# Optimization experiments

Hardware: AMD Instinct MI355X
Metric: run time of the kernel (lower is better)

## Reference

```python
import jax, jax.numpy as jnp
import numpy as np

EMBED_DIM = 128
BATCH = 8
SEQ = 2048


def setup_inputs() -> dict:
    key = jax.random.key(0)
    k1, k2, k3 = jax.random.split(key, 3)
    inputs = jax.random.normal(k1, (BATCH, SEQ, EMBED_DIM), dtype=jnp.float32)
    rotation_params = jax.random.normal(k2, (EMBED_DIM * 3,), dtype=jnp.float32)
    entangle_params = jax.random.normal(k3, (EMBED_DIM,), dtype=jnp.float32)
    return {"inputs": inputs, "rotation_params": rotation_params, "entangle_params": entangle_params}


def reference(inputs, rotation_params, entangle_params):
    d = inputs.shape[-1]
    rot = rotation_params.reshape(d, 3)          # [d, 3]
    ent = entangle_params.reshape(d, 1)          # [d, 1]
    query = inputs @ rot                         # [B, S, 3]
    key = inputs @ ent                           # [B, S, 1]
    # scores: [B, S, S], softmax over last axis
    logits = jnp.einsum('bsk,btk->bst', query, key) / jnp.sqrt(jnp.float32(d))
    scores = jax.nn.softmax(logits, axis=-1)
    return jnp.einsum('bst,btd->bsd', scores, inputs)  # [B, S, d]
```

## Files before the change

### kernel.cpp

```cpp
#include <hip/hip_runtime.h>
#include <cstddef>
#include <cstdint>

#define SS 2048
#define DD 128
#define NB 8

typedef _Float16 half8 __attribute__((ext_vector_type(8)));
typedef __fp16 fp16x2 __attribute__((ext_vector_type(2)));
typedef __attribute__((ext_vector_type(16))) float f32x16;

#if __has_builtin(__builtin_amdgcn_exp2f)
#define EXP2F(x) __builtin_amdgcn_exp2f(x)
#else
#define EXP2F(x) exp2f(x)
#endif

#define WS_A2   0
#define WS_KV   (NB*SS*4)
#define WS_XF   (2*NB*SS*4)
#define BATCH_B (SS*DD*2)
#define WS_NEED (size_t)(WS_XF + (size_t)NB*BATCH_B)
#define WS_KMX  (WS_XF)
#define WS_KMN  (WS_XF + 128)


__global__ __launch_bounds__(256) void prep(
    const float* __restrict__ X, const float* __restrict__ rotp,
    const float* __restrict__ entp, uint8_t* __restrict__ ws, int do_x) {
  __shared__ __align__(16) uint8_t lbuf[128 * 80];
  const int blk = blockIdx.x;
  const int b = blk & 7;
  const int rc = blk >> 3;
  const int tid = threadIdx.x;
  const int d4 = (tid & 31) * 4;
  float* a2out = (float*)(ws + WS_A2);
  float* kout = (float*)(ws + WS_KV);

  const float4 f0 = *reinterpret_cast<const float4*>(rotp + d4 * 3);
  const float4 f1 = *reinterpret_cast<const float4*>(rotp + d4 * 3 + 4);
  const float4 f2 = *reinterpret_cast<const float4*>(rotp + d4 * 3 + 8);
  const float rs0 = f0.x + f0.y + f0.z;
  const float rs1 = f0.w + f1.x + f1.y;
  const float rs2 = f1.z + f1.w + f2.x;
  const float rs3 = f2.y + f2.z + f2.w;
  const float4 e4 = *reinterpret_cast<const float4*>(entp + d4);

#pragma unroll
  for (int rnd = 0; rnd < 4; ++rnd) {
    const int t31 = rnd * 8 + (tid >> 5);
    const int tg = rc * 32 + t31;
    const float4 xv =
        *reinterpret_cast<const float4*>(X + ((size_t)b * SS + tg) * DD + d4);
    float av = xv.x * rs0 + xv.y * rs1 + xv.z * rs2 + xv.w * rs3;
    float kv = xv.x * e4.x + xv.y * e4.y + xv.z * e4.z + xv.w * e4.w;
#pragma unroll
    for (int off = 16; off > 0; off >>= 1) {
      av += __shfl_xor(av, off, 64);
      kv += __shfl_xor(kv, off, 64);
    }
    if ((tid & 31) == 0) {
      a2out[b * SS + tg] = av * (0.08838834764831845f * 1.4426950408889634f);
      kout[b * SS + tg] = kv;
    }
    if (do_x) {
      const float vv[4] = {xv.x, xv.y, xv.z, xv.w};
#pragma unroll
      for (int i = 0; i < 4; ++i)
        *reinterpret_cast<_Float16*>(lbuf + (d4 + i) * 80 + t31 * 2) =
            (_Float16)vv[i];
    }
  }

  if (do_x) {
    __syncthreads();
    const int T = rc >> 2;
    const int wfb = (rc & 3) * 2;
    uint8_t* outb = ws + WS_XF + (size_t)b * BATCH_B + (T * 8 + wfb) * 4096;
    const int nt = tid >> 6;
    const int lane = tid & 63;
    const int hh = lane >> 5;
    const int d = nt * 32 + (lane & 31);
#pragma unroll
    for (int wfl = 0; wfl < 2; ++wfl) {
      const half8 v = *reinterpret_cast<const half8*>(
          lbuf + d * 80 + (wfl * 16 + hh * 8) * 2);
      *reinterpret_cast<half8*>(outb + wfl * 4096 + nt * 1024 + lane * 16) = v;
    }
  }
}

__global__ __launch_bounds__(512, 4) void attn_mfma(
    const uint8_t* __restrict__ ws, float* __restrict__ out) {
  __shared__ float comb[2][32 * 128];
  __shared__ float dl[8 * 32];
  __shared__ float smx[8], smn[8];
  const int tid = threadIdx.x;
  const int w = tid >> 6;
  const int lane = tid & 63;
  const int lm = lane & 31;
  const int h = lane >> 5;
  const int blk = blockIdx.x;
  const int b = blk & 7;
  const int s0 = (blk >> 3) * 32;

  const float* a2 = (const float*)(ws + WS_A2) + b * SS;
  const float* kb = (const float*)(ws + WS_KV) + b * SS;
  const uint8_t* xf = ws + WS_XF + (size_t)b * BATCH_B;

  const float4 k4 = *reinterpret_cast<const float4*>(kb + tid * 4);
  float mx = fmaxf(fmaxf(k4.x, k4.y), fmaxf(k4.z, k4.w));
  float mn = fminf(fminf(k4.x, k4.y), fminf(k4.z, k4.w));
#pragma unroll
  for (int off = 32; off > 0; off >>= 1) {
    mx = fmaxf(mx, __shfl_xor(mx, off, 64));
    mn = fminf(mn, __shfl_xor(mn, off, 64));
  }
  if (lane == 0) { smx[w] = mx; smn[w] = mn; }
  const float ga = a2[s0 + lm];
  __syncthreads();
  mx = smx[0]; mn = smn[0];
#pragma unroll
  for (int q = 1; q < 8; ++q) { mx = fmaxf(mx, smx[q]); mn = fminf(mn, smn[q]); }
  const float gm = fmaxf(ga * mx, ga * mn);
  float gden = 0.0f;

  f32x16 acc[4];
#pragma unroll
  for (int nt = 0; nt < 4; ++nt)
#pragma unroll
    for (int r = 0; r < 16; ++r) acc[nt][r] = 0.0f;

  const uint8_t* wb = xf + w * 4096 + lane * 16;
  const float* kp0 = kb + w * 16 + h * 8;

  half8 bf[4];
#pragma unroll
  for (int nt = 0; nt < 4; ++nt)
    bf[nt] = *reinterpret_cast<const half8*>(wb + nt * 1024);

  for (int T = 0; T < 16; ++T) {
    half8 bn[4];
    if (T < 15) {
      const uint8_t* nb_ = wb + (T + 1) * 32768;
#pragma unroll
      for (int nt = 0; nt < 4; ++nt)
        bn[nt] = *reinterpret_cast<const half8*>(nb_ + nt * 1024);
    }
    const float* kp = kp0 + T * 128;
    const float4 ka = *reinterpret_cast<const float4*>(kp);
    const float4 kc = *reinterpret_cast<const float4*>(kp + 4);
    const float kv8[8] = {ka.x, ka.y, ka.z, ka.w, kc.x, kc.y, kc.z, kc.w};
    float e0[8];
#pragma unroll
    for (int j = 0; j < 8; ++j) {
      e0[j] = EXP2F(fmaf(ga, kv8[j], -gm));
      gden += e0[j];
    }
    union { half8 v; fp16x2 p[4]; } wa;
#pragma unroll
    for (int q = 0; q < 4; ++q)
      wa.p[q] = __builtin_amdgcn_cvt_pkrtz(e0[2 * q], e0[2 * q + 1]);
    __builtin_amdgcn_s_setprio(1);
#pragma unroll
    for (int nt = 0; nt < 4; ++nt)
      acc[nt] = __builtin_amdgcn_mfma_f32_32x32x16_f16(wa.v, bf[nt], acc[nt], 0, 0, 0);
    __builtin_amdgcn_s_setprio(0);
#pragma unroll
    for (int nt = 0; nt < 4; ++nt) bf[nt] = bn[nt];
  }

  gden += __shfl_xor(gden, 32, 64);
  if (lane < 32) dl[w * 32 + lane] = gden;
#pragma unroll
  for (int p = 0; p < 4; ++p) {
    const int grp = w >> 2;
    if ((w & 3) == p) {
      float* cb = comb[grp];
#pragma unroll
      for (int nt = 0; nt < 4; ++nt)
#pragma unroll
        for (int r = 0; r < 16; ++r) {
          const int rr = (r & 3) + 8 * (r >> 2) + 4 * h;
          const int i0 = rr * 128 + nt * 32 + lm;
          if (p == 0) cb[i0] = acc[nt][r];
          else        cb[i0] += acc[nt][r];
        }
    }
    __syncthreads();
  }

  const int r = tid >> 4;
  const int cg = (tid & 15) * 8;
  float den = 0.0f;
#pragma unroll
  for (int q = 0; q < 8; ++q) den += dl[q * 32 + r];
  const float inv = 1.0f / den;
  float* orow = out + ((size_t)b * SS + s0 + r) * DD + cg;
#pragma unroll
  for (int q = 0; q < 2; ++q) {
    const float4 vA = *reinterpret_cast<const float4*>(&comb[0][r * 128 + cg + q * 4]);
    const float4 vB = *reinterpret_cast<const float4*>(&comb[1][r * 128 + cg + q * 4]);
    *reinterpret_cast<float4*>(orow + q * 4) =
        make_float4((vA.x + vB.x) * inv, (vA.y + vB.y) * inv,
                    (vA.z + vB.z) * inv, (vA.w + vB.w) * inv);
  }
}

__global__ __launch_bounds__(256) void kminmax(const float* __restrict__ kvec,
                                               float* __restrict__ kmx,
                                               float* __restrict__ kmn) {
  const int b = blockIdx.x;
  const int tid = threadIdx.x;
  float mx = -1e30f, mn = 1e30f;
  for (int i = tid; i < SS; i += 256) {
    const float v = kvec[b * SS + i];
    mx = fmaxf(mx, v);
    mn = fminf(mn, v);
  }
#pragma unroll
  for (int off = 32; off > 0; off >>= 1) {
    mx = fmaxf(mx, __shfl_xor(mx, off, 64));
    mn = fminf(mn, __shfl_xor(mn, off, 64));
  }
  __shared__ float smx[4], smn[4];
  const int wid = tid >> 6, lane = tid & 63;
  if (lane == 0) { smx[wid] = mx; smn[wid] = mn; }
  __syncthreads();
  if (tid == 0) {
    kmx[b] = fmaxf(fmaxf(smx[0], smx[1]), fmaxf(smx[2], smx[3]));
    kmn[b] = fminf(fminf(smn[0], smn[1]), fminf(smn[2], smn[3]));
  }
}

__global__ __launch_bounds__(256) void attn_main(
    const float* __restrict__ X, const float* __restrict__ a2,
    const float* __restrict__ kvec, const float* __restrict__ kmx,
    const float* __restrict__ kmn, float* __restrict__ out) {
  __shared__ float xs[64 * DD];
  __shared__ float wt[64 * 32];
  __shared__ float denp[8 * 32];
  const int tid = threadIdx.x;
  const int tx = tid & 15;
  const int ty = (tid >> 4) & 3;
  const int tz = tid >> 6;
  const int b = blockIdx.y;
  const int s0 = blockIdx.x * 32;
  const int sg = tid & 31;
  const int tq = tid >> 5;
  const float ga = a2[b * SS + s0 + sg];
  const float gm = fmaxf(ga * kmx[b], ga * kmn[b]);
  float gden = 0.0f;
  float acc[8][8];
#pragma unroll
  for (int r = 0; r < 8; ++r)
#pragma unroll
    for (int c = 0; c < 8; ++c) acc[r][c] = 0.0f;
  const float* xb = X + (size_t)b * SS * DD;
  const float* kb = kvec + b * SS;
  for (int t0 = 0; t0 < SS; t0 += 64) {
    __syncthreads();
#pragma unroll
    for (int rnd = 0; rnd < 8; ++rnd) {
      const int idx = rnd * 1024 + tid * 4;
      *reinterpret_cast<float4*>(xs + idx) =
          *reinterpret_cast<const float4*>(xb + t0 * DD + idx);
    }
#pragma unroll
    for (int j = 0; j < 8; ++j) {
      const float kt = kb[t0 + tq * 8 + j];
      const float wv = exp2f(fmaf(ga, kt, -gm));
      wt[(tq * 8 + j) * 32 + sg] = wv;
      gden += wv;
    }
    __syncthreads();
#pragma unroll 4
    for (int ti = 0; ti < 16; ++ti) {
      const int tl = tz * 16 + ti;
      const float4 x0 = *reinterpret_cast<const float4*>(xs + tl * DD + tx * 8);
      const float4 x1 = *reinterpret_cast<const float4*>(xs + tl * DD + tx * 8 + 4);
      const float4 w0 = *reinterpret_cast<const float4*>(wt + tl * 32 + ty * 8);
      const float4 w1 = *reinterpret_cast<const float4*>(wt + tl * 32 + ty * 8 + 4);
      const float xr[8] = {x0.x, x0.y, x0.z, x0.w, x1.x, x1.y, x1.z, x1.w};
      const float wr[8] = {w0.x, w0.y, w0.z, w0.w, w1.x, w1.y, w1.z, w1.w};
#pragma unroll
      for (int r = 0; r < 8; ++r)
#pragma unroll
        for (int c = 0; c < 8; ++c) acc[r][c] = fmaf(wr[r], xr[c], acc[r][c]);
    }
  }
  __syncthreads();
  denp[tq * 32 + sg] = gden;
  for (int p = 1; p < 4; ++p) {
    __syncthreads();
    if (tz == p) {
#pragma unroll
      for (int r = 0; r < 8; ++r) {
        const int sl = ty * 8 + r;
        *reinterpret_cast<float4*>(xs + sl * DD + tx * 8) =
            make_float4(acc[r][0], acc[r][1], acc[r][2], acc[r][3]);
        *reinterpret_cast<float4*>(xs + sl * DD + tx * 8 + 4) =
            make_float4(acc[r][4], acc[r][5], acc[r][6], acc[r][7]);
      }
    }
    __syncthreads();
    if (tz == 0) {
#pragma unroll
      for (int r = 0; r < 8; ++r) {
        const int sl = ty * 8 + r;
        const float4 v0 = *reinterpret_cast<const float4*>(xs + sl * DD + tx * 8);
        const float4 v1 = *reinterpret_cast<const float4*>(xs + sl * DD + tx * 8 + 4);
        acc[r][0] += v0.x; acc[r][1] += v0.y; acc[r][2] += v0.z; acc[r][3] += v0.w;
        acc[r][4] += v1.x; acc[r][5] += v1.y; acc[r][6] += v1.z; acc[r][7] += v1.w;
      }
    }
  }
  if (tz == 0) {
#pragma unroll
    for (int r = 0; r < 8; ++r) {
      const int sl = ty * 8 + r;
      float den = 0.0f;
#pragma unroll
      for (int q = 0; q < 8; ++q) den += denp[q * 32 + sl];
      const float inv = 1.0f / den;
      float* orow = out + ((size_t)b * SS + s0 + sl) * DD + tx * 8;
      *reinterpret_cast<float4*>(orow) =
          make_float4(acc[r][0] * inv, acc[r][1] * inv, acc[r][2] * inv, acc[r][3] * inv);
      *reinterpret_cast<float4*>(orow + 4) =
          make_float4(acc[r][4] * inv, acc[r][5] * inv, acc[r][6] * inv, acc[r][7] * inv);
    }
  }
}

extern "C" void kernel_launch(void* const* d_in, const int* in_sizes, int n_in,
                              void* d_out, int out_size, void* d_ws, size_t ws_size,
                              hipStream_t stream) {
  const float* X = (const float*)d_in[0];
  const float* rotp = (const float*)d_in[1];
  const float* entp = (const float*)d_in[2];
  float* out = (float*)d_out;
  uint8_t* ws = (uint8_t*)d_ws;

  if (ws_size >= WS_NEED) {
    prep<<<512, 256, 0, stream>>>(X, rotp, entp, ws, 1);
    attn_mfma<<<512, 512, 0, stream>>>((const uint8_t*)ws, out);
  } else {
    float* a2 = (float*)(ws + WS_A2);
    float* kv = (float*)(ws + WS_KV);
    float* kmxp = (float*)(ws + WS_KMX);
    float* kmnp = (float*)(ws + WS_KMN);
    prep<<<512, 256, 0, stream>>>(X, rotp, entp, ws, 0);
    kminmax<<<NB, 256, 0, stream>>>(kv, kmxp, kmnp);
    attn_main<<<dim3(SS / 32, NB), 256, 0, stream>>>(X, a2, kv, kmxp, kmnp, out);
  }
}
```

Measured before the change: 28.46 us.

## Process 64 query rows per block with 16 waves and ping-pong B buffers

The attention kernel now uses 1024-thread blocks that each cover 64 query rows, split as two 32-row halves times eight key-split waves, with half as many blocks. The eight key-split waves for each row half are reduced in one shared buffer instead of two partial buffers summed at the end. The main loop is unrolled by two with alternating A/B fragment registers, so the register-rotation copies go away. Larger blocks mean fewer blocks per CU, longer serial reduction (8 sync steps), and a launch bound of 1024 threads that may limit register allocation.

```diff
diff --git a/kernel.cpp b/kernel.cpp
--- a/kernel.cpp
+++ b/kernel.cpp
@@ -90,38 +90,40 @@
   }
 }
 
-__global__ __launch_bounds__(512, 4) void attn_mfma(
+__global__ __launch_bounds__(1024, 4) void attn_mfma(
     const uint8_t* __restrict__ ws, float* __restrict__ out) {
-  __shared__ float comb[2][32 * 128];
-  __shared__ float dl[8 * 32];
-  __shared__ float smx[8], smn[8];
+  __shared__ float comb[64 * 128];
+  __shared__ float dl[16 * 32];
+  __shared__ float smx[16], smn[16];
   const int tid = threadIdx.x;
   const int w = tid >> 6;
   const int lane = tid & 63;
   const int lm = lane & 31;
   const int h = lane >> 5;
+  const int mh = w >> 3;
+  const int ks = w & 7;
   const int blk = blockIdx.x;
   const int b = blk & 7;
-  const int s0 = (blk >> 3) * 32;
+  const int s0 = (blk >> 3) * 64;
 
   const float* a2 = (const float*)(ws + WS_A2) + b * SS;
   const float* kb = (const float*)(ws + WS_KV) + b * SS;
   const uint8_t* xf = ws + WS_XF + (size_t)b * BATCH_B;
 
-  const float4 k4 = *reinterpret_cast<const float4*>(kb + tid * 4);
-  float mx = fmaxf(fmaxf(k4.x, k4.y), fmaxf(k4.z, k4.w));
-  float mn = fminf(fminf(k4.x, k4.y), fminf(k4.z, k4.w));
+  const float2 k2 = *reinterpret_cast<const float2*>(kb + tid * 2);
+  float mx = fmaxf(k2.x, k2.y);
+  float mn = fminf(k2.x, k2.y);
 #pragma unroll
   for (int off = 32; off > 0; off >>= 1) {
     mx = fmaxf(mx, __shfl_xor(mx, off, 64));
     mn = fminf(mn, __shfl_xor(mn, off, 64));
   }
   if (lane == 0) { smx[w] = mx; smn[w] = mn; }
-  const float ga = a2[s0 + lm];
+  const float ga = a2[s0 + mh * 32 + lm];
   __syncthreads();
   mx = smx[0]; mn = smn[0];
 #pragma unroll
-  for (int q = 1; q < 8; ++q) { mx = fmaxf(mx, smx[q]); mn = fminf(mn, smn[q]); }
+  for (int q = 1; q < 16; ++q) { mx = fmaxf(mx, smx[q]); mn = fminf(mn, smn[q]); }
   const float gm = fmaxf(ga * mx, ga * mn);
   float gden = 0.0f;
 
@@ -131,60 +133,59 @@
 #pragma unroll
     for (int r = 0; r < 16; ++r) acc[nt][r] = 0.0f;
 
-  const uint8_t* wb = xf + w * 4096 + lane * 16;
-  const float* kp0 = kb + w * 16 + h * 8;
-
-  half8 bf[4];
+  const uint8_t* wb = xf + ks * 4096 + lane * 16;
+  const float* kp0 = kb + ks * 16 + h * 8;
+
+  half8 bfA[4], bfB[4];
 #pragma unroll
   for (int nt = 0; nt < 4; ++nt)
-    bf[nt] = *reinterpret_cast<const half8*>(wb + nt * 1024);
-
-  for (int T = 0; T < 16; ++T) {
-    half8 bn[4];
-    if (T < 15) {
-      const uint8_t* nb_ = wb + (T + 1) * 32768;
-#pragma unroll
-      for (int nt = 0; nt < 4; ++nt)
-        bn[nt] = *reinterpret_cast<const half8*>(nb_ + nt * 1024);
-    }
-    const float* kp = kp0 + T * 128;
-    const float4 ka = *reinterpret_cast<const float4*>(kp);
-    const float4 kc = *reinterpret_cast<const float4*>(kp + 4);
-    const float kv8[8] = {ka.x, ka.y, ka.z, ka.w, kc.x, kc.y, kc.z, kc.w};
-    float e0[8];
-#pragma unroll
-    for (int j = 0; j < 8; ++j) {
-      e0[j] = EXP2F(fmaf(ga, kv8[j], -gm));
-      gden += e0[j];
-    }
-    union { half8 v; fp16x2 p[4]; } wa;
-#pragma unroll
-    for (int q = 0; q < 4; ++q)
-      wa.p[q] = __builtin_amdgcn_cvt_pkrtz(e0[2 * q], e0[2 * q + 1]);
-    __builtin_amdgcn_s_setprio(1);
-#pragma unroll
-    for (int nt = 0; nt < 4; ++nt)
-      acc[nt] = __builtin_amdgcn_mfma_f32_32x32x16_f16(wa.v, bf[nt], acc[nt], 0, 0, 0);
-    __builtin_amdgcn_s_setprio(0);
-#pragma unroll
-    for (int nt = 0; nt < 4; ++nt) bf[nt] = bn[nt];
-  }
+    bfA[nt] = *reinterpret_cast<const half8*>(wb + nt * 1024);
+
+#define ABODY(TT, BFP, BFN)                                                   \
+  {                                                                           \
+    if ((TT) + 1 < 16) {                                                      \
+      const uint8_t* nb_ = wb + ((TT) + 1) * 32768;                           \
+      _Pragma("unroll") for (int nt = 0; nt < 4; ++nt)                        \
+          BFN[nt] = *reinterpret_cast<const half8*>(nb_ + nt * 1024);         \
+    }                                                                         \
+    const float* kp = kp0 + (TT) * 128;                                       \
+    const float4 ka = *reinterpret_cast<const float4*>(kp);                   \
+    const float4 kc = *reinterpret_cast<const float4*>(kp + 4);               \
+    const float kv8[8] = {ka.x, ka.y, ka.z, ka.w, kc.x, kc.y, kc.z, kc.w};    \
+    float e0[8];                                                              \
+    _Pragma("unroll") for (int j = 0; j < 8; ++j) {                           \
+      e0[j] = EXP2F(fmaf(ga, kv8[j], -gm));                                   \
+      gden += e0[j];                                                          \
+    }                                                                         \
+    union { half8 v; fp16x2 p[4]; } wa;                                       \
+    _Pragma("unroll") for (int q = 0; q < 4; ++q)                             \
+        wa.p[q] = __builtin_amdgcn_cvt_pkrtz(e0[2 * q], e0[2 * q + 1]);       \
+    __builtin_amdgcn_s_setprio(1);                                            \
+    _Pragma("unroll") for (int nt = 0; nt < 4; ++nt)                          \
+        acc[nt] = __builtin_amdgcn_mfma_f32_32x32x16_f16(wa.v, BFP[nt],       \
+                                                         acc[nt], 0, 0, 0);   \
+    __builtin_amdgcn_s_setprio(0);                                            \
+  }
+
+  for (int T = 0; T < 16; T += 2) {
+    ABODY(T, bfA, bfB);
+    ABODY(T + 1, bfB, bfA);
+  }
+#undef ABODY
 
   gden += __shfl_xor(gden, 32, 64);
   if (lane < 32) dl[w * 32 + lane] = gden;
 #pragma unroll
-  for (int p = 0; p < 4; ++p) {
-    const int grp = w >> 2;
-    if ((w & 3) == p) {
-      float* cb = comb[grp];
+  for (int p = 0; p < 8; ++p) {
+    if (ks == p) {
 #pragma unroll
       for (int nt = 0; nt < 4; ++nt)
 #pragma unroll
         for (int r = 0; r < 16; ++r) {
           const int rr = (r & 3) + 8 * (r >> 2) + 4 * h;
-          const int i0 = rr * 128 + nt * 32 + lm;
-          if (p == 0) cb[i0] = acc[nt][r];
-          else        cb[i0] += acc[nt][r];
+          const int idx = (mh * 32 + rr) * 128 + nt * 32 + lm;
+          if (p == 0) comb[idx] = acc[nt][r];
+          else        comb[idx] += acc[nt][r];
         }
     }
     __syncthreads();
@@ -192,18 +193,17 @@
 
   const int r = tid >> 4;
   const int cg = (tid & 15) * 8;
+  const int rmh = r >> 5, rm = r & 31;
   float den = 0.0f;
 #pragma unroll
-  for (int q = 0; q < 8; ++q) den += dl[q * 32 + r];
+  for (int q = 0; q < 8; ++q) den += dl[(rmh * 8 + q) * 32 + rm];
   const float inv = 1.0f / den;
   float* orow = out + ((size_t)b * SS + s0 + r) * DD + cg;
 #pragma unroll
   for (int q = 0; q < 2; ++q) {
-    const float4 vA = *reinterpret_cast<const float4*>(&comb[0][r * 128 + cg + q * 4]);
-    const float4 vB = *reinterpret_cast<const float4*>(&comb[1][r * 128 + cg + q * 4]);
-    *reinterpret_cast<float4*>(orow + q * 4) =
-        make_float4((vA.x + vB.x) * inv, (vA.y + vB.y) * inv,
-                    (vA.z + vB.z) * inv, (vA.w + vB.w) * inv);
+    float4 v = *reinterpret_cast<const float4*>(&comb[r * 128 + cg + q * 4]);
+    v.x *= inv; v.y *= inv; v.z *= inv; v.w *= inv;
+    *reinterpret_cast<float4*>(orow + q * 4) = v;
   }
 }
 
@@ -343,7 +343,7 @@
 
   if (ws_size >= WS_NEED) {
     prep<<<512, 256, 0, stream>>>(X, rotp, entp, ws, 1);
-    attn_mfma<<<512, 512, 0, stream>>>((const uint8_t*)ws, out);
+    attn_mfma<<<256, 1024, 0, stream>>>((const uint8_t*)ws, out);
   } else {
     float* a2 = (float*)(ws + WS_A2);
     float* kv = (float*)(ws + WS_KV);
```

Result: slower. 32.61 us (+14.6%).

## Stage fp16 x tiles via async global-to-LDS loads with double buffering

Applied to the files above, without the earlier changes.

Replaces the per-wave register prefetch of the fp16 value tiles with `global_load_lds` async copies into a 64KB double-buffered LDS region, read back right before each MFMA. The key vector is also cached in LDS instead of read from global each iteration, and the output-combine buffer now reuses the staging memory. The aim is to take global-load latency and register pressure off the MFMA loop. In exchange it adds a block-wide barrier every iteration and raises LDS use per block to roughly 74KB, which likely prevents the 4 blocks per CU requested in `__launch_bounds__`.

```diff
diff --git a/kernel.cpp b/kernel.cpp
--- a/kernel.cpp
+++ b/kernel.cpp
@@ -90,11 +90,18 @@
   }
 }
 
+typedef __attribute__((address_space(3))) unsigned int lds_u32;
+typedef const __attribute__((address_space(1))) unsigned int glb_u32;
+__device__ __forceinline__ void gload16(const void* g, void* l) {
+  __builtin_amdgcn_global_load_lds((glb_u32*)g, (lds_u32*)l, 16, 0, 0);
+}
+
 __global__ __launch_bounds__(512, 4) void attn_mfma(
     const uint8_t* __restrict__ ws, float* __restrict__ out) {
-  __shared__ float comb[2][32 * 128];
+  __shared__ __align__(16) uint8_t smem[65536];
   __shared__ float dl[8 * 32];
   __shared__ float smx[8], smn[8];
+  __shared__ __align__(16) float kls[SS];
   const int tid = threadIdx.x;
   const int w = tid >> 6;
   const int lane = tid & 63;
@@ -108,7 +115,20 @@
   const float* kb = (const float*)(ws + WS_KV) + b * SS;
   const uint8_t* xf = ws + WS_XF + (size_t)b * BATCH_B;
 
+#define STAGE(Tn, bb)                                                         \
+  {                                                                           \
+    const uint8_t* src_ = xf + (size_t)(Tn) * 32768 + tid * 16;               \
+    uint8_t* dst_ = smem + (bb) + tid * 16;                                   \
+    gload16(src_, dst_);                                                      \
+    gload16(src_ + 8192, dst_ + 8192);                                        \
+    gload16(src_ + 16384, dst_ + 16384);                                      \
+    gload16(src_ + 24576, dst_ + 24576);                                      \
+  }
+
+  STAGE(0, 0);
+
   const float4 k4 = *reinterpret_cast<const float4*>(kb + tid * 4);
+  *reinterpret_cast<float4*>(kls + tid * 4) = k4;
   float mx = fmaxf(fmaxf(k4.x, k4.y), fmaxf(k4.z, k4.w));
   float mn = fminf(fminf(k4.x, k4.y), fminf(k4.z, k4.w));
 #pragma unroll
@@ -131,22 +151,11 @@
 #pragma unroll
     for (int r = 0; r < 16; ++r) acc[nt][r] = 0.0f;
 
-  const uint8_t* wb = xf + w * 4096 + lane * 16;
-  const float* kp0 = kb + w * 16 + h * 8;
-
-  half8 bf[4];
-#pragma unroll
-  for (int nt = 0; nt < 4; ++nt)
-    bf[nt] = *reinterpret_cast<const half8*>(wb + nt * 1024);
+  const float* kp0 = kls + w * 16 + h * 8;
+  int cur = 0;
 
   for (int T = 0; T < 16; ++T) {
-    half8 bn[4];
-    if (T < 15) {
-      const uint8_t* nb_ = wb + (T + 1) * 32768;
-#pragma unroll
-      for (int nt = 0; nt < 4; ++nt)
-        bn[nt] = *reinterpret_cast<const half8*>(nb_ + nt * 1024);
-    }
+    if (T < 15) STAGE(T + 1, (cur ^ 1) << 15);
     const float* kp = kp0 + T * 128;
     const float4 ka = *reinterpret_cast<const float4*>(kp);
     const float4 kc = *reinterpret_cast<const float4*>(kp + 4);
@@ -161,22 +170,27 @@
 #pragma unroll
     for (int q = 0; q < 4; ++q)
       wa.p[q] = __builtin_amdgcn_cvt_pkrtz(e0[2 * q], e0[2 * q + 1]);
+    const uint8_t* bbuf = smem + (cur << 15) + w * 4096 + lane * 16;
     __builtin_amdgcn_s_setprio(1);
 #pragma unroll
-    for (int nt = 0; nt < 4; ++nt)
-      acc[nt] = __builtin_amdgcn_mfma_f32_32x32x16_f16(wa.v, bf[nt], acc[nt], 0, 0, 0);
+    for (int nt = 0; nt < 4; ++nt) {
+      const half8 bf = *reinterpret_cast<const half8*>(bbuf + nt * 1024);
+      acc[nt] = __builtin_amdgcn_mfma_f32_32x32x16_f16(wa.v, bf, acc[nt], 0, 0, 0);
+    }
     __builtin_amdgcn_s_setprio(0);
-#pragma unroll
-    for (int nt = 0; nt < 4; ++nt) bf[nt] = bn[nt];
-  }
-
+    __syncthreads();
+    cur ^= 1;
+  }
+#undef STAGE
+
+  float* comb0 = reinterpret_cast<float*>(smem);
   gden += __shfl_xor(gden, 32, 64);
   if (lane < 32) dl[w * 32 + lane] = gden;
 #pragma unroll
   for (int p = 0; p < 4; ++p) {
     const int grp = w >> 2;
     if ((w & 3) == p) {
-      float* cb = comb[grp];
+      float* cb = comb0 + grp * 32 * 128;
 #pragma unroll
       for (int nt = 0; nt < 4; ++nt)
 #pragma unroll
@@ -199,8 +213,8 @@
   float* orow = out + ((size_t)b * SS + s0 + r) * DD + cg;
 #pragma unroll
   for (int q = 0; q < 2; ++q) {
-    const float4 vA = *reinterpret_cast<const float4*>(&comb[0][r * 128 + cg + q * 4]);
-    const float4 vB = *reinterpret_cast<const float4*>(&comb[1][r * 128 + cg + q * 4]);
+    const float4 vA = *reinterpret_cast<const float4*>(comb0 + r * 128 + cg + q * 4);
+    const float4 vB = *reinterpret_cast<const float4*>(comb0 + 32 * 128 + r * 128 + cg + q * 4);
     *reinterpret_cast<float4*>(orow + q * 4) =
         make_float4((vA.x + vB.x) * inv, (vA.y + vB.y) * inv,
                     (vA.z + vB.z) * inv, (vA.w + vB.w) * inv);
```

Measured after the change: 29.55 us. +3.8%, slower.
